# Performance work log

Measured on AMD Instinct MI355X. Metric: run time of the kernel, lower is better.

Reference implementation:

```python
import jax, jax.numpy as jnp
import numpy as np

N = 50000      # nodes
E = 800000     # edges (avg degree 16)
IN = 256       # in_ft
F1, F2, F3 = 128, 128, 256  # out_ft_list


def _p(k, shape):
    return jax.random.normal(k, shape, dtype=jnp.float32) * 0.05


def setup_inputs() -> dict:
    key = jax.random.key(0)
    ks = jax.random.split(key, 14)
    return {
        "x": jax.random.normal(ks[0], (N, IN), dtype=jnp.float32),
        "edge_index": jax.random.randint(ks[1], (2, E), 0, N, dtype=jnp.int64),
        # proj Linear
        "Wp": _p(ks[2], (IN, F1)), "bp": jnp.zeros((F1,), jnp.float32),
        # SAGEConv1: lin_l (on aggregated neighbors, carries bias) + lin_r (root)
        "Wl1": _p(ks[3], (IN, F1)), "bl1": jnp.zeros((F1,), jnp.float32), "Wr1": _p(ks[4], (IN, F1)),
        # SAGEConv2: input is concat(x_p, h1) -> 2*F1
        "Wl2": _p(ks[5], (2 * F1, F2)), "bl2": jnp.zeros((F2,), jnp.float32), "Wr2": _p(ks[6], (2 * F1, F2)),
        # SAGEConv3: input is concat(x_p, h1, h2) -> 2*F1 + F2
        "Wl3": _p(ks[7], (2 * F1 + F2, F3)), "bl3": jnp.zeros((F3,), jnp.float32), "Wr3": _p(ks[8], (2 * F1 + F2, F3)),
    }


def _sage_mean(h, src, dst, Wl, bl, Wr):
    # PyG SAGEConv(aggr='mean'): out = lin_l(mean_{j in N(i)} h_j) + lin_r(h_i)
    msg = h[src]                                              # [E, F_in]
    summed = jax.ops.segment_sum(msg, dst, num_segments=N)    # [N, F_in]
    deg = jax.ops.segment_sum(jnp.ones((src.shape[0],), h.dtype), dst, num_segments=N)
    mean = summed / jnp.maximum(deg, 1.0)[:, None]
    return mean @ Wl + bl + h @ Wr


def reference(x, edge_index, Wp, bp, Wl1, bl1, Wr1, Wl2, bl2, Wr2, Wl3, bl3, Wr3):
    src, dst = edge_index[0], edge_index[1]  # messages flow src -> dst
    act = jax.nn.relu
    # dropout p=0 (eval) -> identity
    x_p = act(x @ Wp + bp)                                    # [N, F1]
    h1 = act(_sage_mean(x, src, dst, Wl1, bl1, Wr1))          # [N, F1]
    in2 = jnp.concatenate([x_p, h1], axis=1)                  # [N, 2*F1]
    h2 = act(_sage_mean(in2, src, dst, Wl2, bl2, Wr2))        # [N, F2]
    in3 = jnp.concatenate([x_p, h1, h2], axis=1)              # [N, 2*F1+F2]
    h3 = act(_sage_mean(in3, src, dst, Wl3, bl3, Wr3))        # [N, F3]
    return h3
```

## Files before the change

kernel.cpp:

```cpp
#include <hip/hip_runtime.h>

#define MAXDEG 64

typedef _Float16 f16x8 __attribute__((ext_vector_type(8)));
typedef _Float16 f16x4 __attribute__((ext_vector_type(4)));
typedef _Float16 f16x2 __attribute__((ext_vector_type(2)));
typedef float f32x4 __attribute__((ext_vector_type(4)));

struct Blk {
  void* p;
  int mode;
  int relu;
  int ld;
  int c0;
};
struct Epi { Blk b[4]; };


__global__ void build_ell_kernel(const int* __restrict__ ei, int E,
                                 int* __restrict__ deg, int* __restrict__ ell) {
  int e = blockIdx.x * blockDim.x + threadIdx.x;
  if (e >= E) return;
  int s = ei[e];
  int d = ei[E + e];
  int slot = atomicAdd(&deg[d], 1);
  if (slot < MAXDEG) ell[d * MAXDEG + slot] = s;
}

__global__ void invdeg_kernel(const int* __restrict__ deg, float* __restrict__ inv, int N) {
  int i = blockIdx.x * blockDim.x + threadIdx.x;
  if (i < N) inv[i] = 1.0f / (float)(deg[i] > 1 ? deg[i] : 1);
}


__global__ void pack_kernel(const float* __restrict__ Wp, const float* __restrict__ Wl1,
                            const float* __restrict__ Wr1, const float* __restrict__ Wl2,
                            const float* __restrict__ Wr2, const float* __restrict__ Wl3,
                            const float* __restrict__ Wr3,
                            const float* __restrict__ bp, const float* __restrict__ bl1,
                            const float* __restrict__ bl2, const float* __restrict__ bl3,
                            _Float16* __restrict__ Bt1, _Float16* __restrict__ Bt2,
                            _Float16* __restrict__ Bt3,
                            float* __restrict__ bias1, float* __restrict__ bias2,
                            float* __restrict__ bias3) {
  int i = blockIdx.x * blockDim.x + threadIdx.x;
  if (i < 384 * 256) {
    int c = i / 256, k = i % 256;
    float v;
    if (c < 128) v = Wp[k * 128 + c];
    else if (c < 256) v = Wl1[k * 128 + (c - 128)];
    else v = Wr1[k * 128 + (c - 256)];
    Bt1[(long)c * 256 + k] = (_Float16)v;
  }
  if (i < 256 * 256) {
    int c = i / 256, k = i % 256;
    float v = (c < 128) ? Wl2[k * 128 + c] : Wr2[k * 128 + (c - 128)];
    Bt2[(long)c * 256 + k] = (_Float16)v;
  }
  if (i < 512 * 384) {
    int c = i / 384, k = i % 384;
    float v = (c < 256) ? Wl3[k * 256 + c] : Wr3[k * 256 + (c - 256)];
    Bt3[(long)c * 384 + k] = (_Float16)v;
  }
  if (i < 384) bias1[i] = (i < 128) ? bp[i] : ((i < 256) ? 0.f : bl1[i - 256]);
  if (i < 256) bias2[i] = (i < 128) ? 0.f : bl2[i - 128];
  if (i < 512) bias3[i] = (i < 256) ? 0.f : bl3[i - 256];
}


__global__ __launch_bounds__(256)
void convert_kernel(const float* __restrict__ src, long n4, _Float16* __restrict__ dst) {
  long i = (long)blockIdx.x * 256 + threadIdx.x;
  if (i >= n4) return;
  float4 v = *(const float4*)(src + i * 4);
  f16x4 h;
  h[0] = (_Float16)v.x; h[1] = (_Float16)v.y;
  h[2] = (_Float16)v.z; h[3] = (_Float16)v.w;
  *(f16x4*)(dst + i * 4) = h;
}


__global__ __launch_bounds__(256)
void gemm_mfma(const _Float16* __restrict__ A, int lda, int K, int M,
               const _Float16* __restrict__ Bt, int ldb,
               const float* __restrict__ bias,
               const _Float16* __restrict__ zbuf, Epi epi, int ncol) {
  __shared__ _Float16 As[128 * 64];
  __shared__ _Float16 Bs[128 * 64];
  const int t = threadIdx.x;
  const int lane = t & 63;
  const int w = t >> 6;
  const int wr = w >> 1, wc = w & 1;

  int g = blockIdx.x, total = gridDim.x;
  int xcd = g & 7, idx = g >> 3;
  int q8 = total >> 3, r8 = total & 7;
  int logical = (xcd < r8 ? xcd * (q8 + 1) : r8 * (q8 + 1) + (xcd - r8) * q8) + idx;
  int bx = logical / ncol, by = logical - bx * ncol;

  const int row0 = bx * 128;
  const int col0 = by * 128;

  f32x4 acc[4][4];
#pragma unroll
  for (int m = 0; m < 4; m++)
#pragma unroll
    for (int n = 0; n < 4; n++)
#pragma unroll
      for (int j = 0; j < 4; j++) acc[m][n][j] = 0.f;

  const _Float16* srcA[4];
  const _Float16* srcB[4];
  int liveA[4];
  _Float16* ldsA[4];
  _Float16* ldsB[4];
#pragma unroll
  for (int q = 0; q < 4; q++) {
    int s = w * 4 + q;
    int rl = s * 8 + (lane >> 3);
    int c = lane & 7;
    int cs = c ^ (rl & 7);
    long ra = (long)row0 + rl;
    liveA[q] = (ra < M) ? 1 : 0;
    srcA[q] = liveA[q] ? (A + ra * lda + (cs << 3)) : zbuf;
    srcB[q] = Bt + ((long)col0 + rl) * ldb + (cs << 3);
    ldsA[q] = &As[s * 512];
    ldsB[q] = &Bs[s * 512];
  }

  int arow[4], brow[4];
#pragma unroll
  for (int m = 0; m < 4; m++) arow[m] = wr * 64 + m * 16 + (lane & 15);
#pragma unroll
  for (int n = 0; n < 4; n++) brow[n] = wc * 64 + n * 16 + (lane & 15);

  for (int kb = 0; kb < K; kb += 64) {
#pragma unroll
    for (int q = 0; q < 4; q++) {
      const _Float16* pa = srcA[q] + (liveA[q] ? kb : 0);
      __builtin_amdgcn_global_load_lds(
          (const __attribute__((address_space(1))) unsigned int*)pa,
          (__attribute__((address_space(3))) unsigned int*)ldsA[q], 16, 0, 0);
      const _Float16* pb = srcB[q] + kb;
      __builtin_amdgcn_global_load_lds(
          (const __attribute__((address_space(1))) unsigned int*)pb,
          (__attribute__((address_space(3))) unsigned int*)ldsB[q], 16, 0, 0);
    }
    __syncthreads();
#pragma unroll
    for (int kk = 0; kk < 2; kk++) {
      f16x8 af[4], bfr[4];
      int cc = kk * 4 + (lane >> 4);
#pragma unroll
      for (int m = 0; m < 4; m++) {
        int r = arow[m];
        af[m] = *(const f16x8*)&As[r * 64 + ((cc ^ (r & 7)) << 3)];
      }
#pragma unroll
      for (int n = 0; n < 4; n++) {
        int r = brow[n];
        bfr[n] = *(const f16x8*)&Bs[r * 64 + ((cc ^ (r & 7)) << 3)];
      }
#pragma unroll
      for (int m = 0; m < 4; m++)
#pragma unroll
        for (int n = 0; n < 4; n++)
          acc[m][n] = __builtin_amdgcn_mfma_f32_16x16x32_f16(af[m], bfr[n], acc[m][n], 0, 0, 0);
    }
    __syncthreads();
  }

  Blk bk = epi.b[by];
  float bb[4];
#pragma unroll
  for (int n = 0; n < 4; n++) bb[n] = bias[col0 + wc * 64 + n * 16 + (lane & 15)];

#pragma unroll
  for (int m = 0; m < 4; m++) {
#pragma unroll
    for (int j = 0; j < 4; j++) {
      int r = row0 + wr * 64 + m * 16 + (lane >> 4) * 4 + j;
      if (r >= M) continue;
      long base = (long)r * bk.ld + bk.c0 + wc * 64 + (lane & 15);
#pragma unroll
      for (int n = 0; n < 4; n++) {
        float v = acc[m][n][j] + bb[n];
        if (bk.relu) v = fmaxf(v, 0.f);
        if (bk.mode == 0) {
          ((float*)bk.p)[base + n * 16] = v;
        } else {
          ((_Float16*)bk.p)[base + n * 16] = (_Float16)v;
        }
      }
    }
  }
}


template <int V>
__global__ __launch_bounds__(256)
void gather_kernel(const int* __restrict__ ell, const int* __restrict__ deg,
                   const float* __restrict__ inv,
                   const _Float16* __restrict__ y, int yld,
                   const _Float16* __restrict__ zh, int zld, int zc,
                   _Float16* __restrict__ oh, int ohLd, int ohC,
                   float* __restrict__ of, int ofLd, int ofC, int N) {
  typedef _Float16 f16v __attribute__((ext_vector_type(V)));
  int wid = (blockIdx.x * blockDim.x + threadIdx.x) >> 6;
  int lane = threadIdx.x & 63;
  if (wid >= N) return;
  int d = deg[wid];
  if (d > MAXDEG) d = MAXDEG;
  const int* el = ell + wid * MAXDEG;
  const int off = lane * V;

  f16v acc = (f16v)(_Float16)0.f;
  int e = 0;
  for (; e + 8 <= d; e += 8) {
    f16v r0 = *(const f16v*)(y + (size_t)el[e + 0] * yld + off);
    f16v r1 = *(const f16v*)(y + (size_t)el[e + 1] * yld + off);
    f16v r2 = *(const f16v*)(y + (size_t)el[e + 2] * yld + off);
    f16v r3 = *(const f16v*)(y + (size_t)el[e + 3] * yld + off);
    f16v r4 = *(const f16v*)(y + (size_t)el[e + 4] * yld + off);
    f16v r5 = *(const f16v*)(y + (size_t)el[e + 5] * yld + off);
    f16v r6 = *(const f16v*)(y + (size_t)el[e + 6] * yld + off);
    f16v r7 = *(const f16v*)(y + (size_t)el[e + 7] * yld + off);
    acc += ((r0 + r1) + (r2 + r3)) + ((r4 + r5) + (r6 + r7));
  }
  for (; e + 4 <= d; e += 4) {
    f16v r0 = *(const f16v*)(y + (size_t)el[e + 0] * yld + off);
    f16v r1 = *(const f16v*)(y + (size_t)el[e + 1] * yld + off);
    f16v r2 = *(const f16v*)(y + (size_t)el[e + 2] * yld + off);
    f16v r3 = *(const f16v*)(y + (size_t)el[e + 3] * yld + off);
    acc += (r0 + r1) + (r2 + r3);
  }
  for (; e < d; e++) {
    acc += *(const f16v*)(y + (size_t)el[e] * yld + off);
  }

  float sc = inv[wid];
  f16v zv = *(const f16v*)(zh + (size_t)wid * zld + zc + off);
  float h[V];
#pragma unroll
  for (int v = 0; v < V; v++)
    h[v] = fmaxf(fmaf((float)acc[v], sc, (float)zv[v]), 0.f);

  if (of) {
    float* op = of + (size_t)wid * ofLd + ofC + off;
    if (V == 2) {
      float2 w2; w2.x = h[0]; w2.y = h[1];
      *(float2*)op = w2;
    } else {
      float4 w4; w4.x = h[0]; w4.y = h[1]; w4.z = h[2]; w4.w = h[3];
      *(float4*)op = w4;
    }
  }
  if (oh) {
    _Float16* ap = oh + (size_t)wid * ohLd + ohC + off;
    f16v hh;
#pragma unroll
    for (int v = 0; v < V; v++) hh[v] = (_Float16)h[v];
    *(f16v*)ap = hh;
  }
}


extern "C" void kernel_launch(void* const* d_in, const int* in_sizes, int n_in,
                              void* d_out, int out_size, void* d_ws, size_t ws_size,
                              hipStream_t stream) {
  const float* x   = (const float*)d_in[0];
  const int*   ei  = (const int*)d_in[1];
  const float* Wp  = (const float*)d_in[2];
  const float* bp  = (const float*)d_in[3];
  const float* Wl1 = (const float*)d_in[4];
  const float* bl1 = (const float*)d_in[5];
  const float* Wr1 = (const float*)d_in[6];
  const float* Wl2 = (const float*)d_in[7];
  const float* bl2 = (const float*)d_in[8];
  const float* Wr2 = (const float*)d_in[9];
  const float* Wl3 = (const float*)d_in[10];
  const float* bl3 = (const float*)d_in[11];
  const float* Wr3 = (const float*)d_in[12];
  float* out = (float*)d_out;

  const int N = in_sizes[0] / 256;
  const int E = in_sizes[1] / 2;

  char* ws = (char*)d_ws;
  size_t off = 0;
  auto carve = [&](size_t bytes) -> char* {
    char* p = ws + off;
    off = (off + bytes + 255) & ~(size_t)255;
    return p;
  };
  _Float16* A1    = (_Float16*)carve((size_t)N * 256 * 2);
  _Float16* z2    = A1;
  _Float16* z3    = A1;
  _Float16* A23   = (_Float16*)carve((size_t)N * 384 * 2);
  _Float16* ybuf  = (_Float16*)carve((size_t)N * 256 * 2);
  _Float16* z1    = (_Float16*)carve((size_t)N * 128 * 2);
  int*      deg   = (int*)carve((size_t)N * 4);
  float*    inv   = (float*)carve((size_t)N * 4);
  int*      ell   = (int*)carve((size_t)N * MAXDEG * 4);
  _Float16* Bt1   = (_Float16*)carve((size_t)384 * 256 * 2);
  _Float16* Bt2   = (_Float16*)carve((size_t)256 * 256 * 2);
  _Float16* Bt3   = (_Float16*)carve((size_t)512 * 384 * 2);
  float*    bias1 = (float*)carve(384 * 4);
  float*    bias2 = (float*)carve(256 * 4);
  float*    bias3 = (float*)carve(512 * 4);
  _Float16* zbuf  = (_Float16*)carve(256);
  if (off > ws_size) return;

  hipMemsetAsync(deg, 0, (size_t)N * 4, stream);
  hipMemsetAsync(zbuf, 0, 256, stream);
  build_ell_kernel<<<(E + 255) / 256, 256, 0, stream>>>(ei, E, deg, ell);
  invdeg_kernel<<<(N + 255) / 256, 256, 0, stream>>>(deg, inv, N);
  pack_kernel<<<(512 * 384 + 255) / 256, 256, 0, stream>>>(
      Wp, Wl1, Wr1, Wl2, Wr2, Wl3, Wr3, bp, bl1, bl2, bl3,
      Bt1, Bt2, Bt3, bias1, bias2, bias3);

  const int MBG = (N + 127) / 128;
  const int gblocks = (N + 3) / 4;

  convert_kernel<<<(int)(((long)N * 64 + 255) / 256), 256, 0, stream>>>(x, (long)N * 64, A1);
  Epi e1;
  e1.b[0] = { A23,  1, 1, 384, 0 };
  e1.b[1] = { ybuf, 1, 0, 128, 0 };
  e1.b[2] = { z1,   1, 0, 128, 0 };
  e1.b[3] = { nullptr, 0, 0, 0, 0 };
  gemm_mfma<<<MBG * 3, 256, 0, stream>>>(A1, 256, 256, N, Bt1, 256, bias1, zbuf, e1, 3);
  gather_kernel<2><<<gblocks, 256, 0, stream>>>(ell, deg, inv, ybuf, 128, z1, 128, 0,
                                                A23, 384, 128, nullptr, 0, 0, N);

  Epi e2;
  e2.b[0] = { ybuf, 1, 0, 128, 0 };
  e2.b[1] = { z2,   1, 0, 128, 0 };
  e2.b[2] = { nullptr, 0, 0, 0, 0 };
  e2.b[3] = { nullptr, 0, 0, 0, 0 };
  gemm_mfma<<<MBG * 2, 256, 0, stream>>>(A23, 384, 256, N, Bt2, 256, bias2, zbuf, e2, 2);
  gather_kernel<2><<<gblocks, 256, 0, stream>>>(ell, deg, inv, ybuf, 128, z2, 128, 0,
                                                A23, 384, 256, nullptr, 0, 0, N);

  Epi e3;
  e3.b[0] = { ybuf, 1, 0, 256, 0   };
  e3.b[1] = { ybuf, 1, 0, 256, 128 };
  e3.b[2] = { z3,   1, 0, 256, 0   };
  e3.b[3] = { z3,   1, 0, 256, 128 };
  gemm_mfma<<<MBG * 4, 256, 0, stream>>>(A23, 384, 384, N, Bt3, 384, bias3, zbuf, e3, 4);
  gather_kernel<4><<<gblocks, 256, 0, stream>>>(ell, deg, inv, ybuf, 256, z3, 256, 0,
                                                nullptr, 0, 0, out, 256, 0, N);
}
```

Before: 407.1 us.

## Fuse preprocessing kernels, shrink ELL indices to 16-bit, inline inverse degree

Merges ELL construction, the x-to-fp16 conversion and the weight/bias packing into one grid-stride preprocess kernel, which cuts launches. ELL neighbour indices are stored as unsigned short, halving index traffic, and the inverse-degree buffer is dropped in favour of computing it inside the gather. Nontemporal loads and stores are used for the root term and the final output. The 16-bit indices only hold while N fits in 65536, which is true for this N of 50000 but truncates silently for larger graphs.

```diff
diff --git a/kernel.cpp b/kernel.cpp
--- a/kernel.cpp
+++ b/kernel.cpp
@@ -17,66 +17,63 @@
 struct Epi { Blk b[4]; };
 
 
-__global__ void build_ell_kernel(const int* __restrict__ ei, int E,
-                                 int* __restrict__ deg, int* __restrict__ ell) {
-  int e = blockIdx.x * blockDim.x + threadIdx.x;
-  if (e >= E) return;
-  int s = ei[e];
-  int d = ei[E + e];
-  int slot = atomicAdd(&deg[d], 1);
-  if (slot < MAXDEG) ell[d * MAXDEG + slot] = s;
-}
-
-__global__ void invdeg_kernel(const int* __restrict__ deg, float* __restrict__ inv, int N) {
-  int i = blockIdx.x * blockDim.x + threadIdx.x;
-  if (i < N) inv[i] = 1.0f / (float)(deg[i] > 1 ? deg[i] : 1);
-}
-
-
-__global__ void pack_kernel(const float* __restrict__ Wp, const float* __restrict__ Wl1,
-                            const float* __restrict__ Wr1, const float* __restrict__ Wl2,
-                            const float* __restrict__ Wr2, const float* __restrict__ Wl3,
-                            const float* __restrict__ Wr3,
-                            const float* __restrict__ bp, const float* __restrict__ bl1,
-                            const float* __restrict__ bl2, const float* __restrict__ bl3,
-                            _Float16* __restrict__ Bt1, _Float16* __restrict__ Bt2,
-                            _Float16* __restrict__ Bt3,
-                            float* __restrict__ bias1, float* __restrict__ bias2,
-                            float* __restrict__ bias3) {
-  int i = blockIdx.x * blockDim.x + threadIdx.x;
-  if (i < 384 * 256) {
-    int c = i / 256, k = i % 256;
-    float v;
-    if (c < 128) v = Wp[k * 128 + c];
-    else if (c < 256) v = Wl1[k * 128 + (c - 128)];
-    else v = Wr1[k * 128 + (c - 256)];
-    Bt1[(long)c * 256 + k] = (_Float16)v;
-  }
-  if (i < 256 * 256) {
-    int c = i / 256, k = i % 256;
-    float v = (c < 128) ? Wl2[k * 128 + c] : Wr2[k * 128 + (c - 128)];
-    Bt2[(long)c * 256 + k] = (_Float16)v;
-  }
-  if (i < 512 * 384) {
-    int c = i / 384, k = i % 384;
-    float v = (c < 256) ? Wl3[k * 256 + c] : Wr3[k * 256 + (c - 256)];
-    Bt3[(long)c * 384 + k] = (_Float16)v;
-  }
-  if (i < 384) bias1[i] = (i < 128) ? bp[i] : ((i < 256) ? 0.f : bl1[i - 256]);
-  if (i < 256) bias2[i] = (i < 128) ? 0.f : bl2[i - 128];
-  if (i < 512) bias3[i] = (i < 256) ? 0.f : bl3[i - 256];
-}
-
-
 __global__ __launch_bounds__(256)
-void convert_kernel(const float* __restrict__ src, long n4, _Float16* __restrict__ dst) {
-  long i = (long)blockIdx.x * 256 + threadIdx.x;
-  if (i >= n4) return;
-  float4 v = *(const float4*)(src + i * 4);
-  f16x4 h;
-  h[0] = (_Float16)v.x; h[1] = (_Float16)v.y;
-  h[2] = (_Float16)v.z; h[3] = (_Float16)v.w;
-  *(f16x4*)(dst + i * 4) = h;
+void preprocess_kernel(const int* __restrict__ ei, int E, int N,
+                       int* __restrict__ deg, unsigned short* __restrict__ ell,
+                       const float* __restrict__ x, _Float16* __restrict__ A1,
+                       const float* __restrict__ Wp, const float* __restrict__ Wl1,
+                       const float* __restrict__ Wr1, const float* __restrict__ Wl2,
+                       const float* __restrict__ Wr2, const float* __restrict__ Wl3,
+                       const float* __restrict__ Wr3,
+                       const float* __restrict__ bp, const float* __restrict__ bl1,
+                       const float* __restrict__ bl2, const float* __restrict__ bl3,
+                       _Float16* __restrict__ Bt1, _Float16* __restrict__ Bt2,
+                       _Float16* __restrict__ Bt3,
+                       float* __restrict__ bias1, float* __restrict__ bias2,
+                       float* __restrict__ bias3) {
+  const long tid = (long)blockIdx.x * blockDim.x + threadIdx.x;
+  const long stride = (long)gridDim.x * blockDim.x;
+
+  for (long i = tid; i < E; i += stride) {
+    int s = ei[i];
+    int d = ei[E + i];
+    int slot = atomicAdd(&deg[d], 1);
+    if (slot < MAXDEG) ell[(long)d * MAXDEG + slot] = (unsigned short)s;
+  }
+
+  const long n4 = (long)N * 64;
+  for (long i = tid; i < n4; i += stride) {
+    float4 v = *(const float4*)(x + i * 4);
+    f16x4 h;
+    h[0] = (_Float16)v.x; h[1] = (_Float16)v.y;
+    h[2] = (_Float16)v.z; h[3] = (_Float16)v.w;
+    *(f16x4*)(A1 + i * 4) = h;
+  }
+
+  for (long ii = tid; ii < 512 * 384; ii += stride) {
+    int i = (int)ii;
+    if (i < 384 * 256) {
+      int c = i / 256, k = i % 256;
+      float v;
+      if (c < 128) v = Wp[k * 128 + c];
+      else if (c < 256) v = Wl1[k * 128 + (c - 128)];
+      else v = Wr1[k * 128 + (c - 256)];
+      Bt1[(long)c * 256 + k] = (_Float16)v;
+    }
+    if (i < 256 * 256) {
+      int c = i / 256, k = i % 256;
+      float v = (c < 128) ? Wl2[k * 128 + c] : Wr2[k * 128 + (c - 128)];
+      Bt2[(long)c * 256 + k] = (_Float16)v;
+    }
+    {
+      int c = i / 384, k = i % 384;
+      float v = (c < 256) ? Wl3[k * 256 + c] : Wr3[k * 256 + (c - 256)];
+      Bt3[(long)c * 384 + k] = (_Float16)v;
+    }
+    if (i < 384) bias1[i] = (i < 128) ? bp[i] : ((i < 256) ? 0.f : bl1[i - 256]);
+    if (i < 256) bias2[i] = (i < 128) ? 0.f : bl2[i - 128];
+    if (i < 512) bias3[i] = (i < 256) ? 0.f : bl3[i - 256];
+  }
 }
 
 
@@ -199,19 +196,19 @@
 
 template <int V>
 __global__ __launch_bounds__(256)
-void gather_kernel(const int* __restrict__ ell, const int* __restrict__ deg,
-                   const float* __restrict__ inv,
+void gather_kernel(const unsigned short* __restrict__ ell, const int* __restrict__ deg,
                    const _Float16* __restrict__ y, int yld,
                    const _Float16* __restrict__ zh, int zld, int zc,
                    _Float16* __restrict__ oh, int ohLd, int ohC,
                    float* __restrict__ of, int ofLd, int ofC, int N) {
   typedef _Float16 f16v __attribute__((ext_vector_type(V)));
+  typedef float f32v __attribute__((ext_vector_type(V)));
   int wid = (blockIdx.x * blockDim.x + threadIdx.x) >> 6;
   int lane = threadIdx.x & 63;
   if (wid >= N) return;
-  int d = deg[wid];
-  if (d > MAXDEG) d = MAXDEG;
-  const int* el = ell + wid * MAXDEG;
+  int dd = deg[wid];
+  int d = dd > MAXDEG ? MAXDEG : dd;
+  const unsigned short* el = ell + (long)wid * MAXDEG;
   const int off = lane * V;
 
   f16v acc = (f16v)(_Float16)0.f;
@@ -238,8 +235,8 @@
     acc += *(const f16v*)(y + (size_t)el[e] * yld + off);
   }
 
-  float sc = inv[wid];
-  f16v zv = *(const f16v*)(zh + (size_t)wid * zld + zc + off);
+  float sc = 1.0f / (float)(dd > 1 ? dd : 1);
+  f16v zv = __builtin_nontemporal_load((const f16v*)(zh + (size_t)wid * zld + zc + off));
   float h[V];
 #pragma unroll
   for (int v = 0; v < V; v++)
@@ -247,13 +244,10 @@
 
   if (of) {
     float* op = of + (size_t)wid * ofLd + ofC + off;
-    if (V == 2) {
-      float2 w2; w2.x = h[0]; w2.y = h[1];
-      *(float2*)op = w2;
-    } else {
-      float4 w4; w4.x = h[0]; w4.y = h[1]; w4.z = h[2]; w4.w = h[3];
-      *(float4*)op = w4;
-    }
+    f32v wv;
+#pragma unroll
+    for (int v = 0; v < V; v++) wv[v] = h[v];
+    __builtin_nontemporal_store(wv, (f32v*)op);
   }
   if (oh) {
     _Float16* ap = oh + (size_t)wid * ohLd + ohC + off;
@@ -300,8 +294,7 @@
   _Float16* ybuf  = (_Float16*)carve((size_t)N * 256 * 2);
   _Float16* z1    = (_Float16*)carve((size_t)N * 128 * 2);
   int*      deg   = (int*)carve((size_t)N * 4);
-  float*    inv   = (float*)carve((size_t)N * 4);
-  int*      ell   = (int*)carve((size_t)N * MAXDEG * 4);
+  unsigned short* ell = (unsigned short*)carve((size_t)N * MAXDEG * 2);
   _Float16* Bt1   = (_Float16*)carve((size_t)384 * 256 * 2);
   _Float16* Bt2   = (_Float16*)carve((size_t)256 * 256 * 2);
   _Float16* Bt3   = (_Float16*)carve((size_t)512 * 384 * 2);
@@ -313,23 +306,21 @@
 
   hipMemsetAsync(deg, 0, (size_t)N * 4, stream);
   hipMemsetAsync(zbuf, 0, 256, stream);
-  build_ell_kernel<<<(E + 255) / 256, 256, 0, stream>>>(ei, E, deg, ell);
-  invdeg_kernel<<<(N + 255) / 256, 256, 0, stream>>>(deg, inv, N);
-  pack_kernel<<<(512 * 384 + 255) / 256, 256, 0, stream>>>(
+  preprocess_kernel<<<2048, 256, 0, stream>>>(
+      ei, E, N, deg, ell, x, A1,
       Wp, Wl1, Wr1, Wl2, Wr2, Wl3, Wr3, bp, bl1, bl2, bl3,
       Bt1, Bt2, Bt3, bias1, bias2, bias3);
 
   const int MBG = (N + 127) / 128;
   const int gblocks = (N + 3) / 4;
 
-  convert_kernel<<<(int)(((long)N * 64 + 255) / 256), 256, 0, stream>>>(x, (long)N * 64, A1);
   Epi e1;
   e1.b[0] = { A23,  1, 1, 384, 0 };
   e1.b[1] = { ybuf, 1, 0, 128, 0 };
   e1.b[2] = { z1,   1, 0, 128, 0 };
   e1.b[3] = { nullptr, 0, 0, 0, 0 };
   gemm_mfma<<<MBG * 3, 256, 0, stream>>>(A1, 256, 256, N, Bt1, 256, bias1, zbuf, e1, 3);
-  gather_kernel<2><<<gblocks, 256, 0, stream>>>(ell, deg, inv, ybuf, 128, z1, 128, 0,
+  gather_kernel<2><<<gblocks, 256, 0, stream>>>(ell, deg, ybuf, 128, z1, 128, 0,
                                                 A23, 384, 128, nullptr, 0, 0, N);
 
   Epi e2;
@@ -338,7 +329,7 @@
   e2.b[2] = { nullptr, 0, 0, 0, 0 };
   e2.b[3] = { nullptr, 0, 0, 0, 0 };
   gemm_mfma<<<MBG * 2, 256, 0, stream>>>(A23, 384, 256, N, Bt2, 256, bias2, zbuf, e2, 2);
-  gather_kernel<2><<<gblocks, 256, 0, stream>>>(ell, deg, inv, ybuf, 128, z2, 128, 0,
+  gather_kernel<2><<<gblocks, 256, 0, stream>>>(ell, deg, ybuf, 128, z2, 128, 0,
                                                 A23, 384, 256, nullptr, 0, 0, N);
 
   Epi e3;
@@ -347,6 +338,6 @@
   e3.b[2] = { z3,   1, 0, 256, 0   };
   e3.b[3] = { z3,   1, 0, 256, 128 };
   gemm_mfma<<<MBG * 4, 256, 0, stream>>>(A23, 384, 384, N, Bt3, 384, bias3, zbuf, e3, 4);
-  gather_kernel<4><<<gblocks, 256, 0, stream>>>(ell, deg, inv, ybuf, 256, z3, 256, 0,
+  gather_kernel<4><<<gblocks, 256, 0, stream>>>(ell, deg, ybuf, 256, z3, 256, 0,
                                                 nullptr, 0, 0, out, 256, 0, N);
 }
```

Result: faster. 386.8 us (-5.0%).
